# Kernel tuning notes

Measured on AMD Instinct MI355X. Metric: run time of the kernel, lower is better.

Reference implementation:

```python
import jax, jax.numpy as jnp
import numpy as np

LEVEL = 10
S = 2 ** (LEVEL + 1)   # face side (ring size)
HS = S // 2            # half side (rows per face)
B = 2
F = 5                  # five faces of the icosahedral rhombus layout


def setup_inputs() -> dict:
    key = jax.random.key(0)
    ks = jax.random.split(key, 10)
    mk = lambda k, shp: jax.random.normal(k, shp, dtype=jnp.float32)
    return {
        "x": mk(ks[0], (B, F, HS, S)),
        "poles": mk(ks[1], (B, 2, 1)),
        "w_inner": mk(ks[2], (6, HS - 2, S - 2)),
        "w_east": mk(ks[3], (6, HS - 1)),
        "w_cn": mk(ks[4], (6,)),
        "w_ne": mk(ks[5], (6, HS - 2)),
        "w_nne": mk(ks[6], (6,)),
        "w_nw": mk(ks[7], (6, HS - 2)),
        "w_nww": mk(ks[8], (6,)),
        "w_west": mk(ks[9], (6, HS - 1)),
    }


def _wp(face_slice, xi, w):
    # wrap-previous face diff: out[f] = (in[f-1 mod 5] - x[f]) * w
    return (jnp.roll(face_slice, 1, axis=1) - xi) * w


def _wn(face_slice, xi, w):
    # wrap-next face diff: out[f] = (in[f+1 mod 5] - x[f]) * w
    return (jnp.roll(face_slice, -1, axis=1) - xi) * w


def reference(x, poles, w_inner, w_east, w_cn, w_ne, w_nne, w_nw, w_nww, w_west):
    Bb, Ff, hs, s = x.shape
    out = jnp.zeros((Bb, 4, Ff, hs, s), x.dtype)

    # ---- interior patch (all neighbors in-face) ----
    xi = x[:, :, 1:-1, 1:-1]                                  # [B,5,HS-2,S-2]
    d0 = (x[:, :, :-2, :-2] - xi) * w_inner[0]
    d1 = (x[:, :, 2:, 2:] - xi) * w_inner[1]
    d2 = (x[:, :, :-2, 1:-1] - xi) * w_inner[2] + (x[:, :, 1:-1, 2:] - xi) * w_inner[3]
    d3 = (x[:, :, 1:-1, :-2] - xi) * w_inner[4] + (x[:, :, 2:, 1:-1] - xi) * w_inner[5]
    out = out.at[:, :, :, 1:-1, 1:-1].set(jnp.stack([d0, d1, d2, d3], axis=1))

    # ---- east seam: row 0, cols 1:HS ----
    xi = x[:, :, 0, 1:hs]                                     # [B,5,HS-1]
    d0 = _wp(x[:, :, hs - 1, hs:s - 1], xi, w_east[0])
    d1 = (x[:, :, 1, 2:hs + 1] - xi) * w_east[1]
    d2 = _wp(x[:, :, hs - 1, hs + 1:s], xi, w_east[2]) + (x[:, :, 0, 2:hs + 1] - xi) * w_east[3]
    d3 = (x[:, :, 0, 0:hs - 1] - xi) * w_east[4] + (x[:, :, 1, 1:hs] - xi) * w_east[5]
    out = out.at[:, :, :, 0, 1:hs].set(jnp.stack([d0, d1, d2, d3], axis=1))

    # ---- corner-north vertex: row 0, col HS ----
    xi = x[:, :, 0, hs]                                       # [B,5]
    d0 = _wp(x[:, :, hs - 1, s - 1], xi, w_cn[0])
    d1 = (x[:, :, 1, hs + 1] - xi) * w_cn[1]
    d2 = (x[:, :, 0, hs + 1] - xi) * w_cn[2]
    d3 = (x[:, :, 0, hs - 1] - xi) * w_cn[3] + (x[:, :, 1, hs] - xi) * w_cn[4]
    out = out.at[:, :, :, 0, hs].set(jnp.stack([d0, d1, d2, d3], axis=1))

    # ---- north-east seam: row 0, cols HS+1:S-1 ----
    xi = x[:, :, 0, hs + 1:s - 1]                             # [B,5,HS-2]
    d0 = _wp(x[:, :, hs - 2:0:-1, s - 1], xi, w_ne[0]) + _wp(x[:, :, hs - 1:1:-1, s - 1], xi, w_ne[1])
    d1 = (x[:, :, 1, hs + 2:s] - xi) * w_ne[2] + (x[:, :, 1, hs + 1:s - 1] - xi) * w_ne[3]
    d2 = (x[:, :, 0, hs + 2:s] - xi) * w_ne[4]
    d3 = (x[:, :, 0, hs:s - 2] - xi) * w_ne[5]
    out = out.at[:, :, :, 0, hs + 1:s - 1].set(jnp.stack([d0, d1, d2, d3], axis=1))

    # ---- north-north-east corner (touches pole): row 0, col S-1 ----
    xi = x[:, :, 0, s - 1]                                    # [B,5]
    d0 = _wp(x[:, :, 0, s - 1], xi, w_nne[0]) + _wp(x[:, :, 1, s - 1], xi, w_nne[1])
    d1 = _wn(x[:, :, 0, s - 1], xi, w_nne[2]) + (x[:, :, 1, s - 1] - xi) * w_nne[3]
    d2 = (poles[:, 1] - xi) * w_nne[4]
    d3 = (x[:, :, 0, s - 2] - xi) * w_nne[5]
    out = out.at[:, :, :, 0, s - 1].set(jnp.stack([d0, d1, d2, d3], axis=1))

    # ---- north-west seam: rows 1:HS-1, col S-1 ----
    xi = x[:, :, 1:hs - 1, s - 1]                             # [B,5,HS-2]
    d0 = (x[:, :, 0:hs - 2, s - 2] - xi) * w_nw[0]
    d1 = _wn(x[:, :, 0, s - 2:hs:-1], xi, w_nw[1])
    d2 = (x[:, :, 0:hs - 2, s - 1] - xi) * w_nw[2] + _wn(x[:, :, 0, s - 1:hs + 1:-1], xi, w_nw[3])
    d3 = (x[:, :, 1:hs - 1, s - 2] - xi) * w_nw[4] + (x[:, :, 2:hs, s - 1] - xi) * w_nw[5]
    out = out.at[:, :, :, 1:hs - 1, s - 1].set(jnp.stack([d0, d1, d2, d3], axis=1))

    # ---- north-west-west corner: row HS-1, col S-1 ----
    xi = x[:, :, hs - 1, s - 1]                               # [B,5]
    d0 = (x[:, :, hs - 2, s - 2] - xi) * w_nww[0]
    d1 = _wn(x[:, :, 0, hs], xi, w_nww[1])
    d2 = (x[:, :, hs - 2, s - 1] - xi) * w_nww[2] + _wn(x[:, :, 0, hs + 1], xi, w_nww[3])
    d3 = (x[:, :, hs - 1, s - 2] - xi) * w_nww[4] + _wn(x[:, :, 0, hs - 1], xi, w_nww[5])
    out = out.at[:, :, :, hs - 1, s - 1].set(jnp.stack([d0, d1, d2, d3], axis=1))

    # ---- west seam: row HS-1, cols HS:S-1 ----
    xi = x[:, :, hs - 1, hs:s - 1]                            # [B,5,HS-1]
    d0 = (x[:, :, hs - 2, hs - 1:s - 2] - xi) * w_west[0]
    d1 = _wn(x[:, :, 0, 1:hs], xi, w_west[1])
    d2 = (x[:, :, hs - 2, hs:s - 1] - xi) * w_west[2] + (x[:, :, hs - 1, hs + 1:s] - xi) * w_west[3]
    d3 = (x[:, :, hs - 1, hs - 1:s - 2] - xi) * w_west[4] + _wn(x[:, :, 0, 0:hs - 1], xi, w_west[5])
    out = out.at[:, :, :, hs - 1, hs:s - 1].set(jnp.stack([d0, d1, d2, d3], axis=1))

    return out
```

## Files before the change

### kernel.cpp

```cpp
#include <hip/hip_runtime.h>

constexpr int S  = 2048;
constexpr int HS = 1024;
constexpr int B  = 2;
constexpr int F  = 5;
constexpr int PL = HS * S;
constexpr int OD = F * PL;
constexpr int WI = (HS - 2) * (S - 2);

typedef float v4  __attribute__((ext_vector_type(4)));
typedef float v4u __attribute__((ext_vector_type(4), aligned(4)));

__device__ __forceinline__ void st_nt(float* p, v4 v) {
    __builtin_nontemporal_store(v, (v4*)p);
}

__device__ void scalar_point(
    int i, int j,
    const float* __restrict__ x, const float* __restrict__ poles,
    const float* __restrict__ w_inner, const float* __restrict__ w_east,
    const float* __restrict__ w_cn, const float* __restrict__ w_ne,
    const float* __restrict__ w_nne, const float* __restrict__ w_nw,
    const float* __restrict__ w_nww, const float* __restrict__ w_west,
    float* __restrict__ out)
{
    if (j == 0 || (i == HS - 1 && j < HS)) {
        for (int b = 0; b < B; ++b) {
#pragma unroll
            for (int f = 0; f < F; ++f) {
                float* ob = out + b * (4 * OD) + f * PL + i * S + j;
                ob[0] = 0.f; ob[OD] = 0.f; ob[2 * OD] = 0.f; ob[3 * OD] = 0.f;
            }
        }
        return;
    }

    if (i > 0 && i < HS - 1 && j < S - 1) {
        const int wo = (i - 1) * (S - 2) + (j - 1);
        const float w0 = w_inner[wo];
        const float w1 = w_inner[wo + WI];
        const float w2 = w_inner[wo + 2 * WI];
        const float w3 = w_inner[wo + 3 * WI];
        const float w4 = w_inner[wo + 4 * WI];
        const float w5 = w_inner[wo + 5 * WI];
        const int rm = (i - 1) * S + j;
        const int rc = i * S + j;
        const int rp = (i + 1) * S + j;
        for (int b = 0; b < B; ++b) {
#pragma unroll
            for (int f = 0; f < F; ++f) {
                const float* xb = x + (b * F + f) * PL;
                const float xi = xb[rc];
                const float d0 = (xb[rm - 1] - xi) * w0;
                const float d1 = (xb[rp + 1] - xi) * w1;
                const float d2 = (xb[rm] - xi) * w2 + (xb[rc + 1] - xi) * w3;
                const float d3 = (xb[rc - 1] - xi) * w4 + (xb[rp] - xi) * w5;
                float* ob = out + b * (4 * OD) + f * PL + rc;
                ob[0] = d0; ob[OD] = d1; ob[2 * OD] = d2; ob[3 * OD] = d3;
            }
        }
        return;
    }

    if (i == 0) {
        if (j < HS) {
            const int t = j - 1;
            const float w0 = w_east[t];
            const float w1 = w_east[t + (HS - 1)];
            const float w2 = w_east[t + 2 * (HS - 1)];
            const float w3 = w_east[t + 3 * (HS - 1)];
            const float w4 = w_east[t + 4 * (HS - 1)];
            const float w5 = w_east[t + 5 * (HS - 1)];
            for (int b = 0; b < B; ++b) {
#pragma unroll
                for (int f = 0; f < F; ++f) {
                    const int fm = (f == 0) ? F - 1 : f - 1;
                    const float* xb  = x + (b * F + f) * PL;
                    const float* xmb = x + (b * F + fm) * PL;
                    const float xi = xb[j];
                    const float d0 = (xmb[(HS - 1) * S + HS + t] - xi) * w0;
                    const float d1 = (xb[S + 2 + t] - xi) * w1;
                    const float d2 = (xmb[(HS - 1) * S + HS + 1 + t] - xi) * w2
                                   + (xb[2 + t] - xi) * w3;
                    const float d3 = (xb[t] - xi) * w4 + (xb[S + 1 + t] - xi) * w5;
                    float* ob = out + b * (4 * OD) + f * PL + j;
                    ob[0] = d0; ob[OD] = d1; ob[2 * OD] = d2; ob[3 * OD] = d3;
                }
            }
        } else if (j == HS) {
            const float w0 = w_cn[0], w1 = w_cn[1], w2 = w_cn[2], w3 = w_cn[3], w4 = w_cn[4];
            for (int b = 0; b < B; ++b) {
#pragma unroll
                for (int f = 0; f < F; ++f) {
                    const int fm = (f == 0) ? F - 1 : f - 1;
                    const float* xb  = x + (b * F + f) * PL;
                    const float* xmb = x + (b * F + fm) * PL;
                    const float xi = xb[HS];
                    const float d0 = (xmb[(HS - 1) * S + S - 1] - xi) * w0;
                    const float d1 = (xb[S + HS + 1] - xi) * w1;
                    const float d2 = (xb[HS + 1] - xi) * w2;
                    const float d3 = (xb[HS - 1] - xi) * w3 + (xb[S + HS] - xi) * w4;
                    float* ob = out + b * (4 * OD) + f * PL + HS;
                    ob[0] = d0; ob[OD] = d1; ob[2 * OD] = d2; ob[3 * OD] = d3;
                }
            }
        } else if (j < S - 1) {
            const int t = j - HS - 1;
            const float w0 = w_ne[t];
            const float w1 = w_ne[t + (HS - 2)];
            const float w2 = w_ne[t + 2 * (HS - 2)];
            const float w3 = w_ne[t + 3 * (HS - 2)];
            const float w4 = w_ne[t + 4 * (HS - 2)];
            const float w5 = w_ne[t + 5 * (HS - 2)];
            for (int b = 0; b < B; ++b) {
#pragma unroll
                for (int f = 0; f < F; ++f) {
                    const int fm = (f == 0) ? F - 1 : f - 1;
                    const float* xb  = x + (b * F + f) * PL;
                    const float* xmb = x + (b * F + fm) * PL;
                    const float xi = xb[j];
                    const float d0 = (xmb[(HS - 2 - t) * S + S - 1] - xi) * w0
                                   + (xmb[(HS - 1 - t) * S + S - 1] - xi) * w1;
                    const float d1 = (xb[S + HS + 2 + t] - xi) * w2
                                   + (xb[S + HS + 1 + t] - xi) * w3;
                    const float d2 = (xb[HS + 2 + t] - xi) * w4;
                    const float d3 = (xb[HS + t] - xi) * w5;
                    float* ob = out + b * (4 * OD) + f * PL + j;
                    ob[0] = d0; ob[OD] = d1; ob[2 * OD] = d2; ob[3 * OD] = d3;
                }
            }
        } else {
            const float w0 = w_nne[0], w1 = w_nne[1], w2 = w_nne[2],
                        w3 = w_nne[3], w4 = w_nne[4], w5 = w_nne[5];
            for (int b = 0; b < B; ++b) {
#pragma unroll
                for (int f = 0; f < F; ++f) {
                    const int fm = (f == 0) ? F - 1 : f - 1;
                    const int fp = (f == F - 1) ? 0 : f + 1;
                    const float* xb  = x + (b * F + f) * PL;
                    const float* xmb = x + (b * F + fm) * PL;
                    const float* xpb = x + (b * F + fp) * PL;
                    const float xi = xb[S - 1];
                    const float d0 = (xmb[S - 1] - xi) * w0 + (xmb[S + S - 1] - xi) * w1;
                    const float d1 = (xpb[S - 1] - xi) * w2 + (xb[S + S - 1] - xi) * w3;
                    const float d2 = (poles[b * 2 + 1] - xi) * w4;
                    const float d3 = (xb[S - 2] - xi) * w5;
                    float* ob = out + b * (4 * OD) + f * PL + (S - 1);
                    ob[0] = d0; ob[OD] = d1; ob[2 * OD] = d2; ob[3 * OD] = d3;
                }
            }
        }
        return;
    }

    if (i == HS - 1) {
        if (j < S - 1) {
            const int t = j - HS;
            const float w0 = w_west[t];
            const float w1 = w_west[t + (HS - 1)];
            const float w2 = w_west[t + 2 * (HS - 1)];
            const float w3 = w_west[t + 3 * (HS - 1)];
            const float w4 = w_west[t + 4 * (HS - 1)];
            const float w5 = w_west[t + 5 * (HS - 1)];
            for (int b = 0; b < B; ++b) {
#pragma unroll
                for (int f = 0; f < F; ++f) {
                    const int fp = (f == F - 1) ? 0 : f + 1;
                    const float* xb  = x + (b * F + f) * PL;
                    const float* xpb = x + (b * F + fp) * PL;
                    const float xi = xb[(HS - 1) * S + j];
                    const float d0 = (xb[(HS - 2) * S + HS - 1 + t] - xi) * w0;
                    const float d1 = (xpb[1 + t] - xi) * w1;
                    const float d2 = (xb[(HS - 2) * S + HS + t] - xi) * w2
                                   + (xb[(HS - 1) * S + HS + 1 + t] - xi) * w3;
                    const float d3 = (xb[(HS - 1) * S + HS - 1 + t] - xi) * w4
                                   + (xpb[t] - xi) * w5;
                    float* ob = out + b * (4 * OD) + f * PL + (HS - 1) * S + j;
                    ob[0] = d0; ob[OD] = d1; ob[2 * OD] = d2; ob[3 * OD] = d3;
                }
            }
        } else {
            const float w0 = w_nww[0], w1 = w_nww[1], w2 = w_nww[2],
                        w3 = w_nww[3], w4 = w_nww[4], w5 = w_nww[5];
            for (int b = 0; b < B; ++b) {
#pragma unroll
                for (int f = 0; f < F; ++f) {
                    const int fp = (f == F - 1) ? 0 : f + 1;
                    const float* xb  = x + (b * F + f) * PL;
                    const float* xpb = x + (b * F + fp) * PL;
                    const float xi = xb[(HS - 1) * S + S - 1];
                    const float d0 = (xb[(HS - 2) * S + S - 2] - xi) * w0;
                    const float d1 = (xpb[HS] - xi) * w1;
                    const float d2 = (xb[(HS - 2) * S + S - 1] - xi) * w2
                                   + (xpb[HS + 1] - xi) * w3;
                    const float d3 = (xb[(HS - 1) * S + S - 2] - xi) * w4
                                   + (xpb[HS - 1] - xi) * w5;
                    float* ob = out + b * (4 * OD) + f * PL + (HS - 1) * S + (S - 1);
                    ob[0] = d0; ob[OD] = d1; ob[2 * OD] = d2; ob[3 * OD] = d3;
                }
            }
        }
        return;
    }

    {
        const int t = i - 1;
        const float w0 = w_nw[t];
        const float w1 = w_nw[t + (HS - 2)];
        const float w2 = w_nw[t + 2 * (HS - 2)];
        const float w3 = w_nw[t + 3 * (HS - 2)];
        const float w4 = w_nw[t + 4 * (HS - 2)];
        const float w5 = w_nw[t + 5 * (HS - 2)];
        for (int b = 0; b < B; ++b) {
#pragma unroll
            for (int f = 0; f < F; ++f) {
                const int fp = (f == F - 1) ? 0 : f + 1;
                const float* xb  = x + (b * F + f) * PL;
                const float* xpb = x + (b * F + fp) * PL;
                const float xi = xb[i * S + S - 1];
                const float d0 = (xb[(i - 1) * S + S - 2] - xi) * w0;
                const float d1 = (xpb[S - 2 - t] - xi) * w1;
                const float d2 = (xb[(i - 1) * S + S - 1] - xi) * w2
                               + (xpb[S - 1 - t] - xi) * w3;
                const float d3 = (xb[i * S + S - 2] - xi) * w4
                               + (xb[(i + 1) * S + S - 1] - xi) * w5;
                float* ob = out + b * (4 * OD) + f * PL + i * S + (S - 1);
                ob[0] = d0; ob[OD] = d1; ob[2 * OD] = d2; ob[3 * OD] = d3;
            }
        }
    }
}

__global__ __launch_bounds__(256)
void icok(const float* __restrict__ x, const float* __restrict__ poles,
          const float* __restrict__ w_inner, const float* __restrict__ w_east,
          const float* __restrict__ w_cn, const float* __restrict__ w_ne,
          const float* __restrict__ w_nne, const float* __restrict__ w_nw,
          const float* __restrict__ w_nww, const float* __restrict__ w_west,
          float* __restrict__ out)
{
    const int p = blockIdx.x;

    if (p < 2048) {
        const int l = ((p & 7) << 8) | (p >> 3);
        const int i = 1 + (l >> 1);
        if (i > HS - 2) return;
        const int jt = ((l & 1) << 8) | threadIdx.x;
        if (jt == 0 || jt == 511) return;
        const int j0 = jt << 2;

        const int wo = (i - 1) * (S - 2) + (j0 - 1);
        const v4 w0v = *(const v4u*)(w_inner + wo);
        const v4 w1v = *(const v4u*)(w_inner + wo + WI);
        const v4 w2v = *(const v4u*)(w_inner + wo + 2 * WI);
        const v4 w3v = *(const v4u*)(w_inner + wo + 3 * WI);
        const v4 w4v = *(const v4u*)(w_inner + wo + 4 * WI);
        const v4 w5v = *(const v4u*)(w_inner + wo + 5 * WI);

        const int rm = (i - 1) * S + j0;
        const int rc = i * S + j0;
        const int rp = (i + 1) * S + j0;

        for (int b = 0; b < B; ++b) {
#pragma unroll
            for (int f = 0; f < F; ++f) {
                const float* xb = x + (b * F + f) * PL;
                const v4 c = *(const v4*)(xb + rc);
                const v4 m = *(const v4*)(xb + rm);
                const v4 pv = *(const v4*)(xb + rp);
                const float ml = xb[rm - 1];
                const float cl = xb[rc - 1];
                const float cr = xb[rc + 4];
                const float pr = xb[rp + 4];
                const v4 xmm1 = {ml, m.x, m.y, m.z};
                const v4 xpp1 = {pv.y, pv.z, pv.w, pr};
                const v4 xcm1 = {cl, c.x, c.y, c.z};
                const v4 xcp1 = {c.y, c.z, c.w, cr};

                const v4 d0 = (xmm1 - c) * w0v;
                const v4 d1 = (xpp1 - c) * w1v;
                const v4 d2 = (m - c) * w2v + (xcp1 - c) * w3v;
                const v4 d3 = (xcm1 - c) * w4v + (pv - c) * w5v;

                float* ob = out + b * (4 * OD) + f * PL + rc;
                st_nt(ob, d0);
                st_nt(ob + OD, d1);
                st_nt(ob + 2 * OD, d2);
                st_nt(ob + 3 * OD, d3);
            }
        }
        return;
    }

    const int e = (p - 2048) * 256 + threadIdx.x;
    int i, j;
    if (e < 2048)      { i = 0;      j = e; }
    else if (e < 4096) { i = HS - 1; j = e - 2048; }
    else if (e < 4096 + 8 * (HS - 2)) {
        const int t = e - 4096;
        i = 1 + (t >> 3);
        const int c = t & 7;
        j = (c < 4) ? c : (2040 + c);
    } else return;
    scalar_point(i, j, x, poles, w_inner, w_east, w_cn, w_ne, w_nne,
                 w_nw, w_nww, w_west, out);
}

extern "C" void kernel_launch(void* const* d_in, const int* in_sizes, int n_in,
                              void* d_out, int out_size, void* d_ws, size_t ws_size,
                              hipStream_t stream) {
    const float* x       = (const float*)d_in[0];
    const float* poles   = (const float*)d_in[1];
    const float* w_inner = (const float*)d_in[2];
    const float* w_east  = (const float*)d_in[3];
    const float* w_cn    = (const float*)d_in[4];
    const float* w_ne    = (const float*)d_in[5];
    const float* w_nne   = (const float*)d_in[6];
    const float* w_nw    = (const float*)d_in[7];
    const float* w_nww   = (const float*)d_in[8];
    const float* w_west  = (const float*)d_in[9];
    float* out = (float*)d_out;

    dim3 grid(2048 + 48), block(256);
    hipLaunchKernelGGL(icok, grid, block, 0, stream,
                       x, poles, w_inner, w_east, w_cn, w_ne, w_nne, w_nw,
                       w_nww, w_west, out);
}
```

Measured before the change: 459.3 us.

## Split interior work per plane across blocks and use unaligned vector neighbor loads

The interior path now launches one block per (row, half-row, plane) instead of having each thread loop over all 10 batch/face planes, which multiplies the grid by ten. The shifted-neighbor vectors are fetched with unaligned float4 loads in place of scalar edge loads plus shuffles. This aims to raise memory-level parallelism and occupancy for a bandwidth-bound stencil. In exchange, each block reloads the six w_inner weight vectors for every plane, adding weight traffic (likely mostly served from cache), and the unaligned loads may split across cache lines.

```diff
diff --git a/kernel.cpp b/kernel.cpp
--- a/kernel.cpp
+++ b/kernel.cpp
@@ -8,11 +8,17 @@
 constexpr int OD = F * PL;
 constexpr int WI = (HS - 2) * (S - 2);
 
+constexpr int NPLANE = B * F;
+constexpr int INTERIOR_BLOCKS = 8 * 128 * NPLANE * 2;
+
 typedef float v4  __attribute__((ext_vector_type(4)));
 typedef float v4u __attribute__((ext_vector_type(4), aligned(4)));
 
 __device__ __forceinline__ void st_nt(float* p, v4 v) {
     __builtin_nontemporal_store(v, (v4*)p);
+}
+__device__ __forceinline__ v4 ldu(const float* p) {
+    return *(const v4u*)p;
 }
 
 __device__ void scalar_point(
@@ -241,58 +247,56 @@
 {
     const int p = blockIdx.x;
 
-    if (p < 2048) {
-        const int l = ((p & 7) << 8) | (p >> 3);
-        const int i = 1 + (l >> 1);
+    if (p < INTERIOR_BLOCKS) {
+        const int band = p & 7;
+        const int idx  = p >> 3;
+        const int rowb = idx / 20;
+        const int t    = idx - rowb * 20;
+        const int plane = t >> 1;
+        const int half  = t & 1;
+        const int i = band * 128 + rowb + 1;
         if (i > HS - 2) return;
-        const int jt = ((l & 1) << 8) | threadIdx.x;
+        const int jt = (half << 8) | threadIdx.x;
         if (jt == 0 || jt == 511) return;
         const int j0 = jt << 2;
 
         const int wo = (i - 1) * (S - 2) + (j0 - 1);
-        const v4 w0v = *(const v4u*)(w_inner + wo);
-        const v4 w1v = *(const v4u*)(w_inner + wo + WI);
-        const v4 w2v = *(const v4u*)(w_inner + wo + 2 * WI);
-        const v4 w3v = *(const v4u*)(w_inner + wo + 3 * WI);
-        const v4 w4v = *(const v4u*)(w_inner + wo + 4 * WI);
-        const v4 w5v = *(const v4u*)(w_inner + wo + 5 * WI);
+        const v4 w0v = ldu(w_inner + wo);
+        const v4 w1v = ldu(w_inner + wo + WI);
+        const v4 w2v = ldu(w_inner + wo + 2 * WI);
+        const v4 w3v = ldu(w_inner + wo + 3 * WI);
+        const v4 w4v = ldu(w_inner + wo + 4 * WI);
+        const v4 w5v = ldu(w_inner + wo + 5 * WI);
 
         const int rm = (i - 1) * S + j0;
         const int rc = i * S + j0;
         const int rp = (i + 1) * S + j0;
 
-        for (int b = 0; b < B; ++b) {
-#pragma unroll
-            for (int f = 0; f < F; ++f) {
-                const float* xb = x + (b * F + f) * PL;
-                const v4 c = *(const v4*)(xb + rc);
-                const v4 m = *(const v4*)(xb + rm);
-                const v4 pv = *(const v4*)(xb + rp);
-                const float ml = xb[rm - 1];
-                const float cl = xb[rc - 1];
-                const float cr = xb[rc + 4];
-                const float pr = xb[rp + 4];
-                const v4 xmm1 = {ml, m.x, m.y, m.z};
-                const v4 xpp1 = {pv.y, pv.z, pv.w, pr};
-                const v4 xcm1 = {cl, c.x, c.y, c.z};
-                const v4 xcp1 = {c.y, c.z, c.w, cr};
-
-                const v4 d0 = (xmm1 - c) * w0v;
-                const v4 d1 = (xpp1 - c) * w1v;
-                const v4 d2 = (m - c) * w2v + (xcp1 - c) * w3v;
-                const v4 d3 = (xcm1 - c) * w4v + (pv - c) * w5v;
-
-                float* ob = out + b * (4 * OD) + f * PL + rc;
-                st_nt(ob, d0);
-                st_nt(ob + OD, d1);
-                st_nt(ob + 2 * OD, d2);
-                st_nt(ob + 3 * OD, d3);
-            }
-        }
-        return;
-    }
-
-    const int e = (p - 2048) * 256 + threadIdx.x;
+        const float* xb = x + plane * PL;
+        const v4 c   = *(const v4*)(xb + rc);
+        const v4 m   = *(const v4*)(xb + rm);
+        const v4 pv  = *(const v4*)(xb + rp);
+        const v4 mm1 = ldu(xb + rm - 1);
+        const v4 cm1 = ldu(xb + rc - 1);
+        const v4 cp1 = ldu(xb + rc + 1);
+        const v4 pp1 = ldu(xb + rp + 1);
+
+        const v4 d0 = (mm1 - c) * w0v;
+        const v4 d1 = (pp1 - c) * w1v;
+        const v4 d2 = (m - c) * w2v + (cp1 - c) * w3v;
+        const v4 d3 = (cm1 - c) * w4v + (pv - c) * w5v;
+
+        const int bb = (plane >= F) ? 1 : 0;
+        const int ff = plane - bb * F;
+        float* ob = out + bb * (4 * OD) + ff * PL + rc;
+        st_nt(ob, d0);
+        st_nt(ob + OD, d1);
+        st_nt(ob + 2 * OD, d2);
+        st_nt(ob + 3 * OD, d3);
+        return;
+    }
+
+    const int e = (p - INTERIOR_BLOCKS) * 256 + threadIdx.x;
     int i, j;
     if (e < 2048)      { i = 0;      j = e; }
     else if (e < 4096) { i = HS - 1; j = e - 2048; }
@@ -321,7 +325,7 @@
     const float* w_west  = (const float*)d_in[9];
     float* out = (float*)d_out;
 
-    dim3 grid(2048 + 48), block(256);
+    dim3 grid(INTERIOR_BLOCKS + 48), block(256);
     hipLaunchKernelGGL(icok, grid, block, 0, stream,
                        x, poles, w_inner, w_east, w_cn, w_ne, w_nne, w_nw,
                        w_nww, w_west, out);
```

After: 485.0 us. 1.06x slower.

## Process four rows per interior block and move edge blocks first

Applied to the files above, without the earlier changes.

Each interior block now loops over four consecutive rows instead of one, which cuts the grid from 2048 to 512 interior blocks. Consecutive rows share neighbor rows, so x rows may be reused in L2. The edge-handling blocks now come first in the grid, and the w_inner weights are read with nontemporal loads. The row loop is not unrolled, so each block runs longer with less parallelism to hide memory latency.

```diff
diff --git a/kernel.cpp b/kernel.cpp
--- a/kernel.cpp
+++ b/kernel.cpp
@@ -8,11 +8,17 @@
 constexpr int OD = F * PL;
 constexpr int WI = (HS - 2) * (S - 2);
 
+constexpr int EDGE_BLOCKS = 48;
+constexpr int INTERIOR_BLOCKS = 512;
+
 typedef float v4  __attribute__((ext_vector_type(4)));
 typedef float v4u __attribute__((ext_vector_type(4), aligned(4)));
 
 __device__ __forceinline__ void st_nt(float* p, v4 v) {
     __builtin_nontemporal_store(v, (v4*)p);
+}
+__device__ __forceinline__ v4 ldu_nt(const float* p) {
+    return __builtin_nontemporal_load((const v4u*)p);
 }
 
 __device__ void scalar_point(
@@ -241,58 +247,66 @@
 {
     const int p = blockIdx.x;
 
-    if (p < 2048) {
-        const int l = ((p & 7) << 8) | (p >> 3);
-        const int i = 1 + (l >> 1);
-        if (i > HS - 2) return;
-        const int jt = ((l & 1) << 8) | threadIdx.x;
+    if (p >= EDGE_BLOCKS) {
+        const int q    = p - EDGE_BLOCKS;
+        const int band = q & 7;
+        const int idx  = q >> 3;
+        const int g    = (band << 5) + (idx >> 1);
+        const int half = idx & 1;
+        const int jt   = (half << 8) | threadIdx.x;
         if (jt == 0 || jt == 511) return;
         const int j0 = jt << 2;
-
-        const int wo = (i - 1) * (S - 2) + (j0 - 1);
-        const v4 w0v = *(const v4u*)(w_inner + wo);
-        const v4 w1v = *(const v4u*)(w_inner + wo + WI);
-        const v4 w2v = *(const v4u*)(w_inner + wo + 2 * WI);
-        const v4 w3v = *(const v4u*)(w_inner + wo + 3 * WI);
-        const v4 w4v = *(const v4u*)(w_inner + wo + 4 * WI);
-        const v4 w5v = *(const v4u*)(w_inner + wo + 5 * WI);
-
-        const int rm = (i - 1) * S + j0;
-        const int rc = i * S + j0;
-        const int rp = (i + 1) * S + j0;
-
-        for (int b = 0; b < B; ++b) {
-#pragma unroll
-            for (int f = 0; f < F; ++f) {
-                const float* xb = x + (b * F + f) * PL;
-                const v4 c = *(const v4*)(xb + rc);
-                const v4 m = *(const v4*)(xb + rm);
-                const v4 pv = *(const v4*)(xb + rp);
-                const float ml = xb[rm - 1];
-                const float cl = xb[rc - 1];
-                const float cr = xb[rc + 4];
-                const float pr = xb[rp + 4];
-                const v4 xmm1 = {ml, m.x, m.y, m.z};
-                const v4 xpp1 = {pv.y, pv.z, pv.w, pr};
-                const v4 xcm1 = {cl, c.x, c.y, c.z};
-                const v4 xcp1 = {c.y, c.z, c.w, cr};
-
-                const v4 d0 = (xmm1 - c) * w0v;
-                const v4 d1 = (xpp1 - c) * w1v;
-                const v4 d2 = (m - c) * w2v + (xcp1 - c) * w3v;
-                const v4 d3 = (xcm1 - c) * w4v + (pv - c) * w5v;
-
-                float* ob = out + b * (4 * OD) + f * PL + rc;
-                st_nt(ob, d0);
-                st_nt(ob + OD, d1);
-                st_nt(ob + 2 * OD, d2);
-                st_nt(ob + 3 * OD, d3);
-            }
-        }
-        return;
-    }
-
-    const int e = (p - 2048) * 256 + threadIdx.x;
+        const int R0 = (g << 2) + 1;
+
+#pragma unroll 1
+        for (int r = R0; r < R0 + 4; ++r) {
+            if (r > HS - 2) break;
+
+            const int wo = (r - 1) * (S - 2) + (j0 - 1);
+            const v4 w0v = ldu_nt(w_inner + wo);
+            const v4 w1v = ldu_nt(w_inner + wo + WI);
+            const v4 w2v = ldu_nt(w_inner + wo + 2 * WI);
+            const v4 w3v = ldu_nt(w_inner + wo + 3 * WI);
+            const v4 w4v = ldu_nt(w_inner + wo + 4 * WI);
+            const v4 w5v = ldu_nt(w_inner + wo + 5 * WI);
+
+            const int rm = (r - 1) * S + j0;
+            const int rc = r * S + j0;
+            const int rp = (r + 1) * S + j0;
+
+            for (int b = 0; b < B; ++b) {
+#pragma unroll
+                for (int f = 0; f < F; ++f) {
+                    const float* xb = x + (b * F + f) * PL;
+                    const v4 c  = *(const v4*)(xb + rc);
+                    const v4 m  = *(const v4*)(xb + rm);
+                    const v4 pv = *(const v4*)(xb + rp);
+                    const float ml = xb[rm - 1];
+                    const float cl = xb[rc - 1];
+                    const float cr = xb[rc + 4];
+                    const float pr = xb[rp + 4];
+                    const v4 xmm1 = {ml, m.x, m.y, m.z};
+                    const v4 xpp1 = {pv.y, pv.z, pv.w, pr};
+                    const v4 xcm1 = {cl, c.x, c.y, c.z};
+                    const v4 xcp1 = {c.y, c.z, c.w, cr};
+
+                    const v4 d0 = (xmm1 - c) * w0v;
+                    const v4 d1 = (xpp1 - c) * w1v;
+                    const v4 d2 = (m - c) * w2v + (xcp1 - c) * w3v;
+                    const v4 d3 = (xcm1 - c) * w4v + (pv - c) * w5v;
+
+                    float* ob = out + b * (4 * OD) + f * PL + rc;
+                    st_nt(ob, d0);
+                    st_nt(ob + OD, d1);
+                    st_nt(ob + 2 * OD, d2);
+                    st_nt(ob + 3 * OD, d3);
+                }
+            }
+        }
+        return;
+    }
+
+    const int e = p * 256 + threadIdx.x;
     int i, j;
     if (e < 2048)      { i = 0;      j = e; }
     else if (e < 4096) { i = HS - 1; j = e - 2048; }
@@ -321,7 +335,7 @@
     const float* w_west  = (const float*)d_in[9];
     float* out = (float*)d_out;
 
-    dim3 grid(2048 + 48), block(256);
+    dim3 grid(EDGE_BLOCKS + INTERIOR_BLOCKS), block(256);
     hipLaunchKernelGGL(icok, grid, block, 0, stream,
                        x, poles, w_inner, w_east, w_cn, w_ne, w_nne, w_nw,
                        w_nww, w_west, out);
```

After: 476.2 us. +3.7%, slower.
